# Optimization experiments

Hardware: AMD Instinct MI355X
Metric: run time of the kernel (lower is better)

Reference implementation:

```python
import jax, jax.numpy as jnp
import numpy as np

B, L, D, H = 4, 2048, 1024, 16
DK = D // H  # 64


def setup_inputs() -> dict:
    key = jax.random.key(0)
    ks = jax.random.split(key, 8)
    s = 0.05
    return {
        "query": jax.random.normal(ks[0], (B, L, D), jnp.float32),
        "key": jax.random.normal(ks[1], (B, L, D), jnp.float32),
        "value": jax.random.normal(ks[2], (B, L, D), jnp.float32),
        "mask": jnp.ones((B, L, L), jnp.int32),
        "Wq": jax.random.normal(ks[3], (D, DK), jnp.float32) * s,
        "Wk": jax.random.normal(ks[4], (D, DK), jnp.float32) * s,
        "Wv": jax.random.normal(ks[5], (D, DK), jnp.float32) * s,
        "Wo": jax.random.normal(ks[6], (H * DK, D), jnp.float32) * s,
    }


def reference(query, key, value, mask, Wq, Wk, Wv, Wo):
    # Single-head projections (the torch module projects once, then reuses
    # the SAME q/k/v for every head, producing num_heads identical outputs).
    q = jnp.einsum("bld,dk->blk", query, Wq)   # [B, L, DK]
    k = jnp.einsum("bld,dk->blk", key, Wk)
    v = jnp.einsum("bld,dk->blk", value, Wv)
    scale = 1.0 / jnp.sqrt(jnp.asarray(DK, q.dtype))
    scores = jnp.einsum("bqk,bsk->bqs", q, k) * scale  # [B, L, L]
    scores = jnp.where(mask == 0, -jnp.inf, scores)
    p = jax.nn.softmax(scores, axis=-1)
    head = jnp.einsum("bqs,bsk->bqk", p, v)    # [B, L, DK]
    # Concatenation of H identical heads == tile along last dim.
    out = jnp.tile(head, (1, 1, H))             # [B, L, H*DK]
    return jnp.einsum("blh,hd->bld", out, Wo)
```

## Files before the change

### kernel.cpp

```cpp
#include <hip/hip_runtime.h>
#include <hip/hip_bf16.h>

#define Bb 4
#define Ll 2048
#define Dd 1024
#define DKk 64
#define BL (Bb*Ll)
#define G_SPLIT 8

typedef __attribute__((ext_vector_type(4))) float f32x4;
typedef __attribute__((ext_vector_type(8))) short bf16x8;

__device__ __forceinline__ unsigned short f2bf(float x) {
  unsigned int u = __builtin_bit_cast(unsigned int, x);
  u += 0x7fffu + ((u >> 16) & 1u);
  return (unsigned short)(u >> 16);
}
__device__ __forceinline__ unsigned int pack2bf(float a, float b) {
  return (unsigned int)f2bf(a) | ((unsigned int)f2bf(b) << 16);
}

__global__ __launch_bounds__(256)
void prep_kernel(const float* __restrict__ Wq, const float* __restrict__ Wk,
                 const float* __restrict__ Wv, const float* __restrict__ Wo,
                 unsigned short* __restrict__ Wfq, unsigned short* __restrict__ Wfk,
                 unsigned short* __restrict__ Wfv, unsigned short* __restrict__ WoSumT) {
  int idx = blockIdx.x * 256 + threadIdx.x;
  if (idx < 3 * 65536) {
    int which = idx >> 16;
    int r = idx & 65535;
    int n = r & 63, k = r >> 6;
    const float* W = which == 0 ? Wq : (which == 1 ? Wk : Wv);
    unsigned short* Wf = which == 0 ? Wfq : (which == 1 ? Wfk : Wfv);
    const int t = n >> 4, lr = n & 15;
    const int ks = k >> 5, g = (k >> 3) & 3, e = k & 7;
    Wf[(size_t)(((ks * 4 + t) * 4 + g) * 128) + lr * 8 + e] = f2bf(W[(size_t)k * 64 + n]);
  } else {
    int r = idx - 3 * 65536;
    int d = r & 1023, k = r >> 10;
    float s = 0.f;
#pragma unroll
    for (int h = 0; h < 16; ++h) s += Wo[(size_t)(h * 64 + k) * 1024 + d];
    WoSumT[(size_t)d * 64 + k] = f2bf(s);
  }
}

__global__ __launch_bounds__(256)
void projmask_kernel(const float* __restrict__ query, const float* __restrict__ key,
                     const float* __restrict__ value,
                     const unsigned short* __restrict__ Wfq, const unsigned short* __restrict__ Wfk,
                     const unsigned short* __restrict__ Wfv,
                     const int* __restrict__ mask, unsigned long long* __restrict__ BM,
                     unsigned short* __restrict__ Qp, unsigned short* __restrict__ Kf,
                     unsigned short* __restrict__ Vf) {
  __shared__ __align__(16) unsigned short Xl[16 * 1032];

  const int tid = threadIdx.x;

  if (blockIdx.x < 512) {
    const int wid = (blockIdx.x * 256 + tid) >> 6;
    const int lane = tid & 63;
    for (int task = wid; task < BL * 8; task += 2048) {
      const int4 m = *(const int4*)(mask + (size_t)task * 256 + lane * 4);
      unsigned long long b0 = __ballot(m.x != 0);
      unsigned long long b1 = __ballot(m.y != 0);
      unsigned long long b2 = __ballot(m.z != 0);
      unsigned long long b3 = __ballot(m.w != 0);
      unsigned long long v = lane == 0 ? b0 : lane == 1 ? b1 : lane == 2 ? b2 : b3;
      if (lane < 4) BM[(size_t)task * 4 + lane] = v;
    }
    return;
  }

  const int pb = blockIdx.x - 512;
  const int which = pb >> 9;
  const float* X = which == 0 ? query : (which == 1 ? key : value);
  const unsigned short* Wf = which == 0 ? Wfq : (which == 1 ? Wfk : Wfv);
  const int R0 = (pb & 511) * 16;

  const int w = tid >> 6, lane = tid & 63;
  const int g = lane >> 4, lr = lane & 15;

  f32x4 xr[16];
#pragma unroll
  for (int i = 0; i < 8; ++i) {
    int c = tid + 256 * i;
    int row = c >> 7, kc = c & 127;
    const float* src = X + (size_t)(R0 + row) * 1024 + kc * 8;
    xr[2 * i] = *(const f32x4*)src;
    xr[2 * i + 1] = *(const f32x4*)(src + 4);
  }
#pragma unroll
  for (int i = 0; i < 8; ++i) {
    int c = tid + 256 * i;
    int row = c >> 7, kc = c & 127;
    uint4 p;
    p.x = pack2bf(xr[2 * i][0], xr[2 * i][1]);
    p.y = pack2bf(xr[2 * i][2], xr[2 * i][3]);
    p.z = pack2bf(xr[2 * i + 1][0], xr[2 * i + 1][1]);
    p.w = pack2bf(xr[2 * i + 1][2], xr[2 * i + 1][3]);
    *(uint4*)&Xl[row * 1032 + kc * 8] = p;
  }
  __syncthreads();

  f32x4 acc0 = (f32x4){0.f, 0.f, 0.f, 0.f};
  f32x4 acc1 = (f32x4){0.f, 0.f, 0.f, 0.f};
  const unsigned short* xrow = &Xl[lr * 1032 + g * 8];
  const unsigned short* wfb = Wf + (size_t)(w * 4 + g) * 128 + lr * 8;
#pragma unroll
  for (int ks = 0; ks < 32; ks += 2) {
    bf16x8 a0 = *(const bf16x8*)(xrow + ks * 32);
    bf16x8 b0 = *(const bf16x8*)(wfb + (size_t)ks * 2048);
    acc0 = __builtin_amdgcn_mfma_f32_16x16x32_bf16(a0, b0, acc0, 0, 0, 0);
    bf16x8 a1 = *(const bf16x8*)(xrow + (ks + 1) * 32);
    bf16x8 b1 = *(const bf16x8*)(wfb + (size_t)(ks + 1) * 2048);
    acc1 = __builtin_amdgcn_mfma_f32_16x16x32_bf16(a1, b1, acc1, 0, 0, 0);
  }
  f32x4 acc = acc0 + acc1;

  const int dk = w * 16 + lr;
  if (which == 0) {
#pragma unroll
    for (int i = 0; i < 4; ++i)
      Qp[(size_t)(R0 + 4 * g + i) * 64 + dk] = f2bf(acc[i]);
  } else if (which == 1) {
#pragma unroll
    for (int i = 0; i < 4; ++i) {
      const int sg = R0 + 4 * g + i;
      const int b = sg >> 11, sl = sg & 2047;
      const int tile = b * 32 + (sl >> 6), c = (sl >> 4) & 3, lrk = sl & 15;
      Kf[(size_t)tile * 4096 + (c * 8 + (dk >> 3)) * 128 + lrk * 8 + (dk & 7)] = f2bf(acc[i]);
    }
  } else {
#pragma unroll
    for (int i = 0; i < 4; ++i) {
      const int sg = R0 + 4 * g + i;
      const int b = sg >> 11, sl = sg & 2047;
      const int tile = b * 32 + (sl >> 6);
      const int h = (sl >> 5) & 1, g2 = (sl >> 3) & 3, e2 = sl & 7;
      Vf[(size_t)tile * 4096 + ((w * 2 + h) * 4 + g2) * 128 + lr * 8 + e2] = f2bf(acc[i]);
    }
  }
}

__global__ __launch_bounds__(128, 4)
void attn_kernel(const unsigned short* __restrict__ Qp, const unsigned short* __restrict__ Kf,
                 const unsigned short* __restrict__ Vf, const unsigned long long* __restrict__ BM,
                 float* __restrict__ Opart, float* __restrict__ lpart) {
  const int q0 = blockIdx.x * 32;
  const int gy = blockIdx.y;
  const int b = q0 >> 11;
  const int tid = threadIdx.x, lane = tid & 63, w = tid >> 6;
  const int g = lane >> 4, lr = lane & 15;

  const unsigned short* qrow = Qp + (size_t)(q0 + w * 16 + lr) * 64;
  bf16x8 qf0 = *(const bf16x8*)(qrow + g * 8);
  bf16x8 qf1 = *(const bf16x8*)(qrow + 32 + g * 8);

  const unsigned long long* bm = BM + ((size_t)(q0 + w * 16 + lr) * 8 + gy) * 4;
  const unsigned long long W0 = bm[0], W1 = bm[1], W2 = bm[2], W3 = bm[3];

  f32x4 o[4];
#pragma unroll
  for (int t = 0; t < 4; ++t) o[t] = (f32x4){0.f, 0.f, 0.f, 0.f};
  float lsum = 0.f;

  const unsigned short* Kt = Kf + (size_t)(b * 32 + gy * 4) * 4096;
  const unsigned short* Vt = Vf + (size_t)(b * 32 + gy * 4) * 4096;

#pragma unroll
  for (int st = 0; st < 4; ++st) {
    const unsigned short* Kts = Kt + st * 4096;
    const unsigned short* Vts = Vt + st * 4096;

    bf16x8 kf0[4], kf1[4];
#pragma unroll
    for (int c = 0; c < 4; ++c) {
      kf0[c] = *(const bf16x8*)(Kts + (c * 8 + g) * 128 + lr * 8);
      kf1[c] = *(const bf16x8*)(Kts + (c * 8 + 4 + g) * 128 + lr * 8);
    }

    uint2 packs[4];
#pragma unroll
    for (int c = 0; c < 4; ++c) {
      f32x4 a4 = (f32x4){0.f, 0.f, 0.f, 0.f};
      a4 = __builtin_amdgcn_mfma_f32_16x16x32_bf16(kf0[c], qf0, a4, 0, 0, 0);
      a4 = __builtin_amdgcn_mfma_f32_16x16x32_bf16(kf1[c], qf1, a4, 0, 0, 0);
      const int j = st * 16 + 4 * c + g;
      float p0 = ((W0 >> j) & 1) ? __expf(a4[0] * 0.125f) : 0.f;
      float p1 = ((W1 >> j) & 1) ? __expf(a4[1] * 0.125f) : 0.f;
      float p2 = ((W2 >> j) & 1) ? __expf(a4[2] * 0.125f) : 0.f;
      float p3 = ((W3 >> j) & 1) ? __expf(a4[3] * 0.125f) : 0.f;
      lsum += (p0 + p1) + (p2 + p3);
      packs[c].x = pack2bf(p0, p1);
      packs[c].y = pack2bf(p2, p3);
    }

#pragma unroll
    for (int h = 0; h < 2; ++h) {
      const int srcLo = lr + ((g & 1) << 5);
      const int srcHi = srcLo + 16;
      uint2 pl0 = packs[2 * h], pl1 = packs[2 * h + 1];
      unsigned a0x = __shfl((int)pl0.x, srcLo), a0y = __shfl((int)pl0.y, srcLo);
      unsigned a1x = __shfl((int)pl1.x, srcLo), a1y = __shfl((int)pl1.y, srcLo);
      unsigned b0x = __shfl((int)pl0.x, srcHi), b0y = __shfl((int)pl0.y, srcHi);
      unsigned b1x = __shfl((int)pl1.x, srcHi), b1y = __shfl((int)pl1.y, srcHi);
      const bool hisel = ((g >> 1) & 1) != 0;
      uint4 bb;
      bb.x = hisel ? a1x : a0x;
      bb.y = hisel ? a1y : a0y;
      bb.z = hisel ? b1x : b0x;
      bb.w = hisel ? b1y : b0y;
      bf16x8 pb = __builtin_bit_cast(bf16x8, bb);
#pragma unroll
      for (int t = 0; t < 4; ++t) {
        bf16x8 av = *(const bf16x8*)(Vts + ((t * 2 + h) * 4 + g) * 128 + lr * 8);
        o[t] = __builtin_amdgcn_mfma_f32_16x16x32_bf16(av, pb, o[t], 0, 0, 0);
      }
    }
  }

  lsum += __shfl_xor(lsum, 16);
  lsum += __shfl_xor(lsum, 32);

  float* Ob = Opart + ((size_t)(gy * 512 + blockIdx.x * 2 + w) * 4) * 256;
#pragma unroll
  for (int t = 0; t < 4; ++t)
    *(f32x4*)(Ob + (t * 256) + lane * 4) = o[t];
  if (lane < 16)
    lpart[(size_t)gy * BL + q0 + w * 16 + lane] = lsum;
}

__global__ __launch_bounds__(256)
void oproj_kernel(const float* __restrict__ Opart, const float* __restrict__ lpart,
                  const unsigned short* __restrict__ WoSumT, float* __restrict__ out) {
  const int R0 = blockIdx.x * 64;
  const int n0 = blockIdx.y * 256;
  __shared__ __align__(16) unsigned short Hl[64 * 72];
  __shared__ __align__(16) unsigned short Wl[256 * 72];
  const int tid = threadIdx.x, lane = tid & 63, w = tid >> 6;
  const int g = lane >> 4, lr = lane & 15;

#pragma unroll
  for (int i = 0; i < 8; ++i) {
    int c = tid + 256 * i;
    int row = c >> 3, cc = c & 7;
    *(uint4*)&Wl[row * 72 + cc * 8] = *(const uint4*)(WoSumT + (size_t)(n0 + row) * 64 + cc * 8);
  }

  {
    const int t = w;
#pragma unroll
    for (int j = 0; j < 4; ++j) {
      const int rg = (R0 >> 4) + j;
      const int q = rg * 16 + lr;
      f32x4 s = (f32x4){0.f, 0.f, 0.f, 0.f};
      float l = 0.f;
#pragma unroll
      for (int gg = 0; gg < G_SPLIT; ++gg) {
        f32x4 a = *(const f32x4*)(Opart + ((size_t)((gg * 512 + rg) * 4 + t)) * 256 + lane * 4);
        s[0] += a[0]; s[1] += a[1]; s[2] += a[2]; s[3] += a[3];
        l += lpart[(size_t)gg * BL + q];
      }
      const float inv = 1.f / l;
      uint2 pv;
      pv.x = pack2bf(s[0] * inv, s[1] * inv);
      pv.y = pack2bf(s[2] * inv, s[3] * inv);
      *(uint2*)&Hl[(j * 16 + lr) * 72 + t * 16 + g * 4] = pv;
    }
  }
  __syncthreads();

  f32x4 acc[16];
#pragma unroll
  for (int t = 0; t < 16; ++t) acc[t] = (f32x4){0.f, 0.f, 0.f, 0.f};
#pragma unroll
  for (int kh = 0; kh < 2; ++kh) {
    bf16x8 a = *(const bf16x8*)&Hl[(w * 16 + lr) * 72 + kh * 32 + g * 8];
#pragma unroll
    for (int t = 0; t < 16; ++t) {
      bf16x8 bb = *(const bf16x8*)&Wl[(t * 16 + lr) * 72 + kh * 32 + g * 8];
      acc[t] = __builtin_amdgcn_mfma_f32_16x16x32_bf16(a, bb, acc[t], 0, 0, 0);
    }
  }
  float* ob = out + (size_t)(R0 + w * 16 + g * 4) * 1024 + n0 + lr;
#pragma unroll
  for (int t = 0; t < 16; ++t)
#pragma unroll
    for (int i = 0; i < 4; ++i)
      ob[(size_t)i * 1024 + t * 16] = acc[t][i];
}

extern "C" void kernel_launch(void* const* d_in, const int* in_sizes, int n_in,
                              void* d_out, int out_size, void* d_ws, size_t ws_size,
                              hipStream_t stream) {
  const float* query = (const float*)d_in[0];
  const float* key   = (const float*)d_in[1];
  const float* value = (const float*)d_in[2];
  const int*   mask  = (const int*)d_in[3];
  const float* Wq    = (const float*)d_in[4];
  const float* Wk    = (const float*)d_in[5];
  const float* Wv    = (const float*)d_in[6];
  const float* Wo    = (const float*)d_in[7];
  float* out = (float*)d_out;

  unsigned short* Qp   = (unsigned short*)d_ws;
  unsigned short* Kf   = Qp + (size_t)BL * 64;
  unsigned short* Vf   = Kf + (size_t)BL * 64;
  unsigned short* Wfq  = Vf + (size_t)BL * 64;
  unsigned short* Wfk  = Wfq + 65536;
  unsigned short* Wfv  = Wfk + 65536;
  unsigned short* WoSumT = Wfv + 65536;
  float* lpart = (float*)(WoSumT + 65536);
  float* Opart = lpart + (size_t)G_SPLIT * BL;
  unsigned long long* BM = (unsigned long long*)(Opart + (size_t)G_SPLIT * BL * 64);

  hipLaunchKernelGGL(prep_kernel, dim3(1024), dim3(256), 0, stream,
                     Wq, Wk, Wv, Wo, Wfq, Wfk, Wfv, WoSumT);
  hipLaunchKernelGGL(projmask_kernel, dim3(2048), dim3(256), 0, stream,
                     query, key, value, Wfq, Wfk, Wfv, mask, BM, Qp, Kf, Vf);
  hipLaunchKernelGGL(attn_kernel, dim3(BL / 32, G_SPLIT), dim3(128), 0, stream,
                     Qp, Kf, Vf, BM, Opart, lpart);
  hipLaunchKernelGGL(oproj_kernel, dim3(128, 4), dim3(256), 0, stream,
                     Opart, lpart, WoSumT, out);
}
```

Baseline: 67.70 us.

## Fold mask bit-packing into projection blocks with early-issued mask loads

```diff
diff --git a/kernel.cpp b/kernel.cpp
--- a/kernel.cpp
+++ b/kernel.cpp
@@ -7,6 +7,7 @@
 #define DKk 64
 #define BL (Bb*Ll)
 #define G_SPLIT 8
+#define NMW 11
 
 typedef __attribute__((ext_vector_type(4))) float f32x4;
 typedef __attribute__((ext_vector_type(8))) short bf16x8;
@@ -56,30 +57,22 @@
   __shared__ __align__(16) unsigned short Xl[16 * 1032];
 
   const int tid = threadIdx.x;
-
-  if (blockIdx.x < 512) {
-    const int wid = (blockIdx.x * 256 + tid) >> 6;
-    const int lane = tid & 63;
-    for (int task = wid; task < BL * 8; task += 2048) {
-      const int4 m = *(const int4*)(mask + (size_t)task * 256 + lane * 4);
-      unsigned long long b0 = __ballot(m.x != 0);
-      unsigned long long b1 = __ballot(m.y != 0);
-      unsigned long long b2 = __ballot(m.z != 0);
-      unsigned long long b3 = __ballot(m.w != 0);
-      unsigned long long v = lane == 0 ? b0 : lane == 1 ? b1 : lane == 2 ? b2 : b3;
-      if (lane < 4) BM[(size_t)task * 4 + lane] = v;
-    }
-    return;
-  }
-
-  const int pb = blockIdx.x - 512;
-  const int which = pb >> 9;
+  const int which = blockIdx.x >> 9;
   const float* X = which == 0 ? query : (which == 1 ? key : value);
   const unsigned short* Wf = which == 0 ? Wfq : (which == 1 ? Wfk : Wfv);
-  const int R0 = (pb & 511) * 16;
+  const int R0 = (blockIdx.x & 511) * 16;
 
   const int w = tid >> 6, lane = tid & 63;
   const int g = lane >> 4, lr = lane & 15;
+  const int wid = blockIdx.x * 4 + w;
+
+  int4 mreg[NMW];
+#pragma unroll
+  for (int j = 0; j < NMW; ++j) {
+    int task = wid + j * 6144;
+    int ct = task < BL * 8 ? task : 0;
+    mreg[j] = *(const int4*)(mask + (size_t)ct * 256 + lane * 4);
+  }
 
   f32x4 xr[16];
 #pragma unroll
@@ -139,6 +132,19 @@
       const int tile = b * 32 + (sl >> 6);
       const int h = (sl >> 5) & 1, g2 = (sl >> 3) & 3, e2 = sl & 7;
       Vf[(size_t)tile * 4096 + ((w * 2 + h) * 4 + g2) * 128 + lr * 8 + e2] = f2bf(acc[i]);
+    }
+  }
+
+#pragma unroll
+  for (int j = 0; j < NMW; ++j) {
+    const int task = wid + j * 6144;
+    if (task < BL * 8) {
+      unsigned long long c0 = __ballot(mreg[j].x != 0);
+      unsigned long long c1 = __ballot(mreg[j].y != 0);
+      unsigned long long c2 = __ballot(mreg[j].z != 0);
+      unsigned long long c3 = __ballot(mreg[j].w != 0);
+      unsigned long long v = lane == 0 ? c0 : lane == 1 ? c1 : lane == 2 ? c2 : c3;
+      if (lane < 4) BM[(size_t)task * 4 + lane] = v;
     }
   }
 }
@@ -317,7 +323,7 @@
 
   hipLaunchKernelGGL(prep_kernel, dim3(1024), dim3(256), 0, stream,
                      Wq, Wk, Wv, Wo, Wfq, Wfk, Wfv, WoSumT);
-  hipLaunchKernelGGL(projmask_kernel, dim3(2048), dim3(256), 0, stream,
+  hipLaunchKernelGGL(projmask_kernel, dim3(1536), dim3(256), 0, stream,
                      query, key, value, Wfq, Wfk, Wfv, mask, BM, Qp, Kf, Vf);
   hipLaunchKernelGGL(attn_kernel, dim3(BL / 32, G_SPLIT), dim3(128), 0, stream,
                      Qp, Kf, Vf, BM, Opart, lpart);
```

Measured after the change: 70.22 us. 3.7% more time.
